# Kernel tuning notes

Measured on AMD Instinct MI355X. Metric: run time of the kernel, lower is better.

The kernel has to match this reference:

```python
import jax, jax.numpy as jnp
import numpy as np

M, K, N = 4096, 4096, 4096

def setup_inputs() -> dict:
    key = jax.random.key(0)
    k1, k2, k3, k4 = jax.random.split(key, 4)
    a = jax.random.randint(k1, (M, K), 0, 127, dtype=jnp.int32)  # int8 activations
    b = jax.random.randint(k2, (N, K), 0, 127, dtype=jnp.int32)  # int8 weights [N,K]
    alpha_row = jax.random.uniform(k3, (M, 1), dtype=jnp.float32)  # per-row dequant scale
    alpha_col = jax.random.uniform(k4, (1, N), dtype=jnp.float32)  # per-col dequant scale
    return {"a": a, "b": b, "alpha_row": alpha_row, "alpha_col": alpha_col}

def reference(a, b, alpha_row, alpha_col):
    # x = a_fp32 @ b_fp32^T  -> [M, N]
    x = jnp.matmul(a.astype(jnp.float32), b.astype(jnp.float32).T)
    # outer-product dequant scale [M,1] x [1,N] -> [M,N], fused multiply
    out = x * (alpha_row * alpha_col)
    return out.astype(jnp.float16)
```

## Files before the change

kernel.cpp:

```cpp
#include <hip/hip_runtime.h>


constexpr int MD = 4096, ND = 4096, KD = 4096;
constexpr int BM = 256, BN = 256, BKB = 128;
constexpr int NT = KD / BKB;
constexpr int TB = BM * BKB;

using i32x4 = __attribute__((ext_vector_type(4))) int;

#define VMCNT0() asm volatile("s_waitcnt vmcnt(0)" ::: "memory")
#define VMCNT2() asm volatile("s_waitcnt vmcnt(2)" ::: "memory")
#define VMCNT4() asm volatile("s_waitcnt vmcnt(4)" ::: "memory")
#define BAR() __builtin_amdgcn_s_barrier()

__global__ __launch_bounds__(256) void pack_i8(const int* __restrict__ in,
                                               char* __restrict__ out) {
  const size_t t = (size_t)blockIdx.x * 256 + threadIdx.x;
  const int4* p = (const int4*)in + t * 4;
  int4 v0 = p[0], v1 = p[1], v2 = p[2], v3 = p[3];
  int4 o;
  o.x = v0.x | (v0.y << 8) | (v0.z << 16) | (v0.w << 24);
  o.y = v1.x | (v1.y << 8) | (v1.z << 16) | (v1.w << 24);
  o.z = v2.x | (v2.y << 8) | (v2.z << 16) | (v2.w << 24);
  o.w = v3.x | (v3.y << 8) | (v3.z << 16) | (v3.w << 24);
  ((int4*)out)[t] = o;
}

__device__ inline void load16_lds(const char* g, char* l) {
  __builtin_amdgcn_global_load_lds(
      (const __attribute__((address_space(1))) void*)g,
      (__attribute__((address_space(3))) void*)l, 16, 0, 0);
}

__device__ inline float f16_sat(float v) {
  v = fminf(v, 65504.0f);
  return (float)(_Float16)v;
}

__global__ __launch_bounds__(512, 2) void gemm_i8w8(
    const char* __restrict__ A, const char* __restrict__ B,
    const float* __restrict__ arow, const float* __restrict__ acol,
    float* __restrict__ out) {
  __shared__ char sA[2][TB];
  __shared__ char sB[2][TB];

  const int tid = threadIdx.x;
  const int wv = tid >> 6;
  const int lane = tid & 63;

  const int bid = blockIdx.x;
  const int wg = (bid & 7) * 32 + (bid >> 3);
  const int brow = wg >> 4;
  const int bcol = wg & 15;

  const int wrow = (wv >> 2) * 128;
  const int wcol = (wv & 3) * 64;

  i32x4 acc[8][4] = {};

  const int lr = lane >> 3;
  const int lsg = ((lane & 7) ^ lr) * 16;
  const int q0 = wv * 2, q1 = wv * 2 + 1;
  const int rA0 = (q0 >> 3) * 128 + (q0 & 7) * 8;
  const int rA1 = (q1 >> 3) * 128 + (q1 & 7) * 8;
  const int rB0 = (q0 >> 2) * 64 + (q0 & 3) * 8;
  const int rB1 = (q1 >> 2) * 64 + (q1 & 3) * 8;
  const char* srcA0 = A + (size_t)(brow * BM + rA0 + lr) * KD + lsg;
  const char* srcA1 = A + (size_t)(brow * BM + rA1 + lr) * KD + lsg;
  const char* srcB0 = B + (size_t)(bcol * BN + rB0 + lr) * KD + lsg;
  const char* srcB1 = B + (size_t)(bcol * BN + rB1 + lr) * KD + lsg;
  const size_t skip32 = (size_t)32 * KD, skip64 = (size_t)64 * KD;

  auto STAGE_U1 = [&](int nb, size_t kb) {
    load16_lds(srcA0 + kb, sA[nb] + rA0 * BKB);
    load16_lds(srcA1 + kb, sA[nb] + rA1 * BKB);
    load16_lds(srcB0 + kb, sB[nb] + rB0 * BKB);
    load16_lds(srcB1 + kb, sB[nb] + rB1 * BKB);
  };
  auto STAGE_U2 = [&](int nb, size_t kb) {
    load16_lds(srcB0 + skip32 + kb, sB[nb] + (rB0 + 32) * BKB);
    load16_lds(srcB1 + skip32 + kb, sB[nb] + (rB1 + 32) * BKB);
  };
  auto STAGE_U3 = [&](int nb, size_t kb) {
    load16_lds(srcA0 + skip64 + kb, sA[nb] + (rA0 + 64) * BKB);
    load16_lds(srcA1 + skip64 + kb, sA[nb] + (rA1 + 64) * BKB);
  };

  const int r = lane & 15;
  const int s0 = (((lane >> 4) + 0) ^ (r & 7)) * 16;
  const int s1 = (((lane >> 4) + 4) ^ (r & 7)) * 16;
  const int aBase = (wrow + r) * BKB;
  const int bBase = (wcol + r) * BKB;

  STAGE_U1(0, 0);
  STAGE_U2(0, 0);
  STAGE_U3(0, 0);
  VMCNT4();
  BAR();

  i32x4 af[4][2], bf[4][2];

  for (int i = 0; i < NT; ++i) {
    const int cb = i & 1, nb = cb ^ 1;
    const size_t kb = (size_t)(i + 1) * BKB;
    const char* pa = sA[cb] + aBase;
    const char* pb = sB[cb] + bBase;
    const bool more = (i + 1) < NT;

#pragma unroll
    for (int m = 0; m < 4; ++m) {
      af[m][0] = *(const i32x4*)(pa + m * 2048 + s0);
      af[m][1] = *(const i32x4*)(pa + m * 2048 + s1);
    }
#pragma unroll
    for (int n = 0; n < 2; ++n) {
      bf[n][0] = *(const i32x4*)(pb + n * 2048 + s0);
      bf[n][1] = *(const i32x4*)(pb + n * 2048 + s1);
    }
    BAR();
    __builtin_amdgcn_s_setprio(1);
#pragma unroll
    for (int m = 0; m < 4; ++m)
#pragma unroll
      for (int n = 0; n < 2; ++n) {
        acc[m][n] = __builtin_amdgcn_mfma_i32_16x16x64_i8(af[m][0], bf[n][0],
                                                          acc[m][n], 0, 0, 0);
        acc[m][n] = __builtin_amdgcn_mfma_i32_16x16x64_i8(af[m][1], bf[n][1],
                                                          acc[m][n], 0, 0, 0);
      }
    __builtin_amdgcn_s_setprio(0);
    VMCNT2();
    BAR();

#pragma unroll
    for (int n = 2; n < 4; ++n) {
      bf[n][0] = *(const i32x4*)(pb + n * 2048 + s0);
      bf[n][1] = *(const i32x4*)(pb + n * 2048 + s1);
    }
    if (more) STAGE_U1(nb, kb);
    BAR();
    __builtin_amdgcn_s_setprio(1);
#pragma unroll
    for (int m = 0; m < 4; ++m)
#pragma unroll
      for (int n = 2; n < 4; ++n) {
        acc[m][n] = __builtin_amdgcn_mfma_i32_16x16x64_i8(af[m][0], bf[n][0],
                                                          acc[m][n], 0, 0, 0);
        acc[m][n] = __builtin_amdgcn_mfma_i32_16x16x64_i8(af[m][1], bf[n][1],
                                                          acc[m][n], 0, 0, 0);
      }
    __builtin_amdgcn_s_setprio(0);
    if (more) {
      VMCNT4();
    } else {
      VMCNT0();
    }
    BAR();

#pragma unroll
    for (int m = 0; m < 4; ++m) {
      af[m][0] = *(const i32x4*)(pa + (m + 4) * 2048 + s0);
      af[m][1] = *(const i32x4*)(pa + (m + 4) * 2048 + s1);
    }
    if (more) STAGE_U2(nb, kb);
    BAR();
    __builtin_amdgcn_s_setprio(1);
#pragma unroll
    for (int m = 0; m < 4; ++m)
#pragma unroll
      for (int n = 0; n < 2; ++n) {
        acc[m + 4][n] = __builtin_amdgcn_mfma_i32_16x16x64_i8(
            af[m][0], bf[n][0], acc[m + 4][n], 0, 0, 0);
        acc[m + 4][n] = __builtin_amdgcn_mfma_i32_16x16x64_i8(
            af[m][1], bf[n][1], acc[m + 4][n], 0, 0, 0);
      }
    __builtin_amdgcn_s_setprio(0);
    BAR();

    if (more) STAGE_U3(nb, kb);
    BAR();
    __builtin_amdgcn_s_setprio(1);
#pragma unroll
    for (int m = 0; m < 4; ++m)
#pragma unroll
      for (int n = 2; n < 4; ++n) {
        acc[m + 4][n] = __builtin_amdgcn_mfma_i32_16x16x64_i8(
            af[m][0], bf[n][0], acc[m + 4][n], 0, 0, 0);
        acc[m + 4][n] = __builtin_amdgcn_mfma_i32_16x16x64_i8(
            af[m][1], bf[n][1], acc[m + 4][n], 0, 0, 0);
      }
    __builtin_amdgcn_s_setprio(0);
    VMCNT4();
    BAR();
  }

  const int orow0 = brow * BM + wrow + ((lane >> 4) << 2);
  const int ocol0 = bcol * BN + wcol + (lane & 15);
#pragma unroll
  for (int m = 0; m < 8; ++m) {
    const int rb = orow0 + m * 16;
    const float ar0 = arow[rb + 0], ar1 = arow[rb + 1];
    const float ar2 = arow[rb + 2], ar3 = arow[rb + 3];
#pragma unroll
    for (int n = 0; n < 4; ++n) {
      const int col = ocol0 + n * 16;
      const float ac = acol[col];
      out[(size_t)(rb + 0) * ND + col] = f16_sat((float)acc[m][n][0] * (ar0 * ac));
      out[(size_t)(rb + 1) * ND + col] = f16_sat((float)acc[m][n][1] * (ar1 * ac));
      out[(size_t)(rb + 2) * ND + col] = f16_sat((float)acc[m][n][2] * (ar2 * ac));
      out[(size_t)(rb + 3) * ND + col] = f16_sat((float)acc[m][n][3] * (ar3 * ac));
    }
  }
}

extern "C" void kernel_launch(void* const* d_in, const int* in_sizes, int n_in,
                              void* d_out, int out_size, void* d_ws, size_t ws_size,
                              hipStream_t stream) {
  const int* a = (const int*)d_in[0];
  const int* b = (const int*)d_in[1];
  const float* arow = (const float*)d_in[2];
  const float* acol = (const float*)d_in[3];
  float* out = (float*)d_out;

  char* pa = (char*)d_ws;
  char* pb = pa + (size_t)MD * KD;

  const int packBlocks = (int)(((size_t)MD * KD) / (16 * 256));
  pack_i8<<<packBlocks, 256, 0, stream>>>(a, pa);
  pack_i8<<<packBlocks, 256, 0, stream>>>(b, pb);

  const int grid = (MD / BM) * (ND / BN);
  gemm_i8w8<<<grid, 512, 0, stream>>>(pa, pb, arow, acol, out);
}
```

Baseline: 104.0 us.

## Restructure GEMM main loop to prefetch next-tile fragments and cut barriers

Reorders the four-phase MFMA loop so the next K-tile's A and B fragments are read from LDS at the end of the current iteration. Global-to-LDS loads are regrouped: the first and second B halves issue together after the first MFMA block, and vmcnt thresholds are adjusted to match. The aim is to overlap LDS reads with compute and remove some barriers per iteration. The cost is more live fragment registers and tighter wait-count reasoning, which could break correctness if a count is wrong.

```diff
diff --git a/kernel.cpp b/kernel.cpp
--- a/kernel.cpp
+++ b/kernel.cpp
@@ -8,9 +8,7 @@
 
 using i32x4 = __attribute__((ext_vector_type(4))) int;
 
-#define VMCNT0() asm volatile("s_waitcnt vmcnt(0)" ::: "memory")
-#define VMCNT2() asm volatile("s_waitcnt vmcnt(2)" ::: "memory")
-#define VMCNT4() asm volatile("s_waitcnt vmcnt(4)" ::: "memory")
+#define VMCNT(n) asm volatile("s_waitcnt vmcnt(" #n ")" ::: "memory")
 #define BAR() __builtin_amdgcn_s_barrier()
 
 __global__ __launch_bounds__(256) void pack_i8(const int* __restrict__ in,
@@ -71,17 +69,17 @@
   const char* srcB1 = B + (size_t)(bcol * BN + rB1 + lr) * KD + lsg;
   const size_t skip32 = (size_t)32 * KD, skip64 = (size_t)64 * KD;
 
-  auto STAGE_U1 = [&](int nb, size_t kb) {
+  auto STAGE_UE = [&](int nb, size_t kb) {
     load16_lds(srcA0 + kb, sA[nb] + rA0 * BKB);
     load16_lds(srcA1 + kb, sA[nb] + rA1 * BKB);
     load16_lds(srcB0 + kb, sB[nb] + rB0 * BKB);
     load16_lds(srcB1 + kb, sB[nb] + rB1 * BKB);
   };
-  auto STAGE_U2 = [&](int nb, size_t kb) {
+  auto STAGE_UB1 = [&](int nb, size_t kb) {
     load16_lds(srcB0 + skip32 + kb, sB[nb] + (rB0 + 32) * BKB);
     load16_lds(srcB1 + skip32 + kb, sB[nb] + (rB1 + 32) * BKB);
   };
-  auto STAGE_U3 = [&](int nb, size_t kb) {
+  auto STAGE_UA1 = [&](int nb, size_t kb) {
     load16_lds(srcA0 + skip64 + kb, sA[nb] + (rA0 + 64) * BKB);
     load16_lds(srcA1 + skip64 + kb, sA[nb] + (rA1 + 64) * BKB);
   };
@@ -92,105 +90,115 @@
   const int aBase = (wrow + r) * BKB;
   const int bBase = (wcol + r) * BKB;
 
-  STAGE_U1(0, 0);
-  STAGE_U2(0, 0);
-  STAGE_U3(0, 0);
-  VMCNT4();
+  STAGE_UE(0, 0);
+  STAGE_UB1(0, 0);
+  STAGE_UA1(0, 0);
+  VMCNT(2);
   BAR();
 
-  i32x4 af[4][2], bf[4][2];
+  i32x4 af[4][2], bf0[2][2], bf1[2][2];
+#pragma unroll
+  for (int m = 0; m < 4; ++m) {
+    af[m][0] = *(const i32x4*)(sA[0] + aBase + m * 2048 + s0);
+    af[m][1] = *(const i32x4*)(sA[0] + aBase + m * 2048 + s1);
+  }
+#pragma unroll
+  for (int n = 0; n < 2; ++n) {
+    bf0[n][0] = *(const i32x4*)(sB[0] + bBase + n * 2048 + s0);
+    bf0[n][1] = *(const i32x4*)(sB[0] + bBase + n * 2048 + s1);
+  }
 
   for (int i = 0; i < NT; ++i) {
     const int cb = i & 1, nb = cb ^ 1;
     const size_t kb = (size_t)(i + 1) * BKB;
     const char* pa = sA[cb] + aBase;
     const char* pb = sB[cb] + bBase;
+    const char* pan = sA[nb] + aBase;
+    const char* pbn = sB[nb] + bBase;
     const bool more = (i + 1) < NT;
 
 #pragma unroll
-    for (int m = 0; m < 4; ++m) {
-      af[m][0] = *(const i32x4*)(pa + m * 2048 + s0);
-      af[m][1] = *(const i32x4*)(pa + m * 2048 + s1);
-    }
-#pragma unroll
     for (int n = 0; n < 2; ++n) {
-      bf[n][0] = *(const i32x4*)(pb + n * 2048 + s0);
-      bf[n][1] = *(const i32x4*)(pb + n * 2048 + s1);
-    }
-    BAR();
-    __builtin_amdgcn_s_setprio(1);
-#pragma unroll
-    for (int m = 0; m < 4; ++m)
-#pragma unroll
-      for (int n = 0; n < 2; ++n) {
-        acc[m][n] = __builtin_amdgcn_mfma_i32_16x16x64_i8(af[m][0], bf[n][0],
+      bf1[n][0] = *(const i32x4*)(pb + (n + 2) * 2048 + s0);
+      bf1[n][1] = *(const i32x4*)(pb + (n + 2) * 2048 + s1);
+    }
+    __builtin_amdgcn_s_setprio(1);
+#pragma unroll
+    for (int m = 0; m < 4; ++m)
+#pragma unroll
+      for (int n = 0; n < 2; ++n) {
+        acc[m][n] = __builtin_amdgcn_mfma_i32_16x16x64_i8(af[m][0], bf0[n][0],
                                                           acc[m][n], 0, 0, 0);
-        acc[m][n] = __builtin_amdgcn_mfma_i32_16x16x64_i8(af[m][1], bf[n][1],
+        acc[m][n] = __builtin_amdgcn_mfma_i32_16x16x64_i8(af[m][1], bf0[n][1],
                                                           acc[m][n], 0, 0, 0);
       }
     __builtin_amdgcn_s_setprio(0);
-    VMCNT2();
-    BAR();
-
-#pragma unroll
-    for (int n = 2; n < 4; ++n) {
-      bf[n][0] = *(const i32x4*)(pb + n * 2048 + s0);
-      bf[n][1] = *(const i32x4*)(pb + n * 2048 + s1);
-    }
-    if (more) STAGE_U1(nb, kb);
-    BAR();
-    __builtin_amdgcn_s_setprio(1);
-#pragma unroll
-    for (int m = 0; m < 4; ++m)
-#pragma unroll
-      for (int n = 2; n < 4; ++n) {
-        acc[m][n] = __builtin_amdgcn_mfma_i32_16x16x64_i8(af[m][0], bf[n][0],
-                                                          acc[m][n], 0, 0, 0);
-        acc[m][n] = __builtin_amdgcn_mfma_i32_16x16x64_i8(af[m][1], bf[n][1],
-                                                          acc[m][n], 0, 0, 0);
-      }
-    __builtin_amdgcn_s_setprio(0);
     if (more) {
-      VMCNT4();
+      STAGE_UE(nb, kb);
+      STAGE_UB1(nb, kb);
+      VMCNT(6);
     } else {
-      VMCNT0();
-    }
-    BAR();
-
+      VMCNT(0);
+    }
+    BAR();
+
+    __builtin_amdgcn_s_setprio(1);
+#pragma unroll
+    for (int m = 0; m < 4; ++m)
+#pragma unroll
+      for (int n = 0; n < 2; ++n) {
+        acc[m][n + 2] = __builtin_amdgcn_mfma_i32_16x16x64_i8(
+            af[m][0], bf1[n][0], acc[m][n + 2], 0, 0, 0);
+        acc[m][n + 2] = __builtin_amdgcn_mfma_i32_16x16x64_i8(
+            af[m][1], bf1[n][1], acc[m][n + 2], 0, 0, 0);
+      }
+    __builtin_amdgcn_s_setprio(0);
 #pragma unroll
     for (int m = 0; m < 4; ++m) {
       af[m][0] = *(const i32x4*)(pa + (m + 4) * 2048 + s0);
       af[m][1] = *(const i32x4*)(pa + (m + 4) * 2048 + s1);
     }
-    if (more) STAGE_U2(nb, kb);
-    BAR();
+    if (more) STAGE_UA1(nb, kb);
+    BAR();
+
     __builtin_amdgcn_s_setprio(1);
 #pragma unroll
     for (int m = 0; m < 4; ++m)
 #pragma unroll
       for (int n = 0; n < 2; ++n) {
         acc[m + 4][n] = __builtin_amdgcn_mfma_i32_16x16x64_i8(
-            af[m][0], bf[n][0], acc[m + 4][n], 0, 0, 0);
+            af[m][0], bf0[n][0], acc[m + 4][n], 0, 0, 0);
         acc[m + 4][n] = __builtin_amdgcn_mfma_i32_16x16x64_i8(
-            af[m][1], bf[n][1], acc[m + 4][n], 0, 0, 0);
-      }
-    __builtin_amdgcn_s_setprio(0);
-    BAR();
-
-    if (more) STAGE_U3(nb, kb);
-    BAR();
-    __builtin_amdgcn_s_setprio(1);
-#pragma unroll
-    for (int m = 0; m < 4; ++m)
-#pragma unroll
-      for (int n = 2; n < 4; ++n) {
-        acc[m + 4][n] = __builtin_amdgcn_mfma_i32_16x16x64_i8(
-            af[m][0], bf[n][0], acc[m + 4][n], 0, 0, 0);
-        acc[m + 4][n] = __builtin_amdgcn_mfma_i32_16x16x64_i8(
-            af[m][1], bf[n][1], acc[m + 4][n], 0, 0, 0);
-      }
-    __builtin_amdgcn_s_setprio(0);
-    VMCNT4();
+            af[m][1], bf0[n][1], acc[m + 4][n], 0, 0, 0);
+      }
+    __builtin_amdgcn_s_setprio(0);
+    VMCNT(4);
+    BAR();
+
+    __builtin_amdgcn_s_setprio(1);
+#pragma unroll
+    for (int m = 0; m < 4; ++m)
+#pragma unroll
+      for (int n = 0; n < 2; ++n) {
+        acc[m + 4][n + 2] = __builtin_amdgcn_mfma_i32_16x16x64_i8(
+            af[m][0], bf1[n][0], acc[m + 4][n + 2], 0, 0, 0);
+        acc[m + 4][n + 2] = __builtin_amdgcn_mfma_i32_16x16x64_i8(
+            af[m][1], bf1[n][1], acc[m + 4][n + 2], 0, 0, 0);
+      }
+    __builtin_amdgcn_s_setprio(0);
+    if (more) {
+#pragma unroll
+      for (int m = 0; m < 4; ++m) {
+        af[m][0] = *(const i32x4*)(pan + m * 2048 + s0);
+        af[m][1] = *(const i32x4*)(pan + m * 2048 + s1);
+      }
+#pragma unroll
+      for (int n = 0; n < 2; ++n) {
+        bf0[n][0] = *(const i32x4*)(pbn + n * 2048 + s0);
+        bf0[n][1] = *(const i32x4*)(pbn + n * 2048 + s1);
+      }
+    }
+    VMCNT(2);
     BAR();
   }
 
```

New measurement: 90.09 us. -13.4%, faster.
